# Performance work log

Hardware: AMD Instinct MI355X
Metric: run time of the kernel (lower is better)

## Reference

```python
import jax, jax.numpy as jnp
import numpy as np

N, E, G = 50000, 500000, 32
H, D = 4, 40  # heads, per-head dim; hidden = H*D = 160
HID, JK = H * D, 2 * H * D  # 160, 320


def setup_inputs() -> dict:
    key = jax.random.key(0)
    ks = jax.random.split(key, 32)
    s = 0.05
    inp = {
        'x': jax.random.normal(ks[0], (N, 5), jnp.float32),
        'edge_index': jax.random.randint(ks[1], (2, E), 0, N, jnp.int32).astype(jnp.int64),
        'edge_attr': jax.random.normal(ks[2], (E, 4), jnp.float32),
        'batch': jnp.sort(jax.random.randint(ks[3], (N,), 0, G, jnp.int32)).astype(jnp.int64),
        'W_in': jax.random.normal(ks[4], (5, HID), jnp.float32) * s,
        'b_in': jnp.zeros((HID,), jnp.float32),
        'Wq': jax.random.normal(ks[5], (2, HID, HID), jnp.float32) * s,
        'bq': jnp.zeros((2, HID), jnp.float32),
        'Wk': jax.random.normal(ks[6], (2, HID, HID), jnp.float32) * s,
        'bk': jnp.zeros((2, HID), jnp.float32),
        'Wv': jax.random.normal(ks[7], (2, HID, HID), jnp.float32) * s,
        'bv': jnp.zeros((2, HID), jnp.float32),
        'We': jax.random.normal(ks[8], (2, 4, HID), jnp.float32) * s,
        'be': jnp.zeros((2, HID), jnp.float32),
        'Wskip': jax.random.normal(ks[9], (2, HID, HID), jnp.float32) * s,
        'bskip': jnp.zeros((2, HID), jnp.float32),
        'Wbeta': jax.random.normal(ks[10], (2, 3 * HID, 1), jnp.float32) * s,
        'Wg1': jax.random.normal(ks[11], (JK, JK // 2), jnp.float32) * s,
        'bg1': jnp.zeros((JK // 2,), jnp.float32),
        'Wg2': jax.random.normal(ks[12], (JK // 2, 1), jnp.float32) * s,
        'bg2': jnp.zeros((1,), jnp.float32),
        'Wh1': jax.random.normal(ks[13], (JK, JK), jnp.float32) * s,
        'bh1': jnp.zeros((JK,), jnp.float32),
        'Wh2': jax.random.normal(ks[14], (JK, 6), jnp.float32) * s,
        'bh2': jnp.zeros((6,), jnp.float32),
    }
    return inp


def _transformer_conv(h, src, dst, edge_attr, Wq, bq, Wk, bk, Wv, bv, We, be, Wskip, bskip, Wbeta):
    n = h.shape[0]
    q = (h @ Wq + bq).reshape(n, H, D)
    k = (h @ Wk + bk).reshape(n, H, D)
    v = (h @ Wv + bv).reshape(n, H, D)
    e = (edge_attr @ We + be).reshape(-1, H, D)   # [E,H,D]
    k_e = k[src] + e                              # key with edge feature
    v_e = v[src] + e                              # value with edge feature
    alpha = jnp.einsum('ehd,ehd->eh', q[dst], k_e) / jnp.sqrt(jnp.float32(D))  # [E,H]
    # segment softmax over incoming edges of each destination node
    amax = jax.ops.segment_max(alpha, dst, num_segments=n)
    ex = jnp.exp(alpha - amax[dst])
    denom = jax.ops.segment_sum(ex, dst, num_segments=n)
    a = ex / denom[dst]                           # [E,H]
    out = jax.ops.segment_sum(v_e * a[..., None], dst, num_segments=n).reshape(n, H * D)
    # beta gate with skip connection
    r = h @ Wskip + bskip
    beta = jax.nn.sigmoid(jnp.concatenate([out, r, out - r], axis=-1) @ Wbeta)  # [n,1]
    return beta * r + (1.0 - beta) * out


def reference(x, edge_index, edge_attr, batch, W_in, b_in, Wq, bq, Wk, bk, Wv, bv,
              We, be, Wskip, bskip, Wbeta, Wg1, bg1, Wg2, bg2, Wh1, bh1, Wh2, bh2):
    src, dst = edge_index[0], edge_index[1]
    h = x @ W_in + b_in
    xs = []
    for l in range(2):
        h = _transformer_conv(h, src, dst, edge_attr, Wq[l], bq[l], Wk[l], bk[l],
                              Wv[l], bv[l], We[l], be[l], Wskip[l], bskip[l], Wbeta[l])
        xs.append(h)
    xc = jnp.concatenate(xs, axis=-1)             # JumpingKnowledge 'cat' -> [N,320]
    # AttentionalAggregation: gate MLP + segment softmax over graphs
    gate = jax.nn.relu(xc @ Wg1 + bg1) @ Wg2 + bg2  # [N,1]
    gmax = jax.ops.segment_max(gate, batch, num_segments=G)
    ge = jnp.exp(gate - gmax[batch])
    gden = jax.ops.segment_sum(ge, batch, num_segments=G)
    att = ge / gden[batch]
    pooled = jax.ops.segment_sum(att * xc, batch, num_segments=G)  # [G,320]
    out = jax.nn.relu(pooled @ Wh1 + bh1) @ Wh2 + bh2              # [G,6]
    return out.reshape(-1, 2, 3)
```

## Files before the change

kernel.cpp:

```cpp
#include <hip/hip_runtime.h>
#include <math.h>
#include <stddef.h>

#define NHEAD 4
#define DHEAD 40
#define HIDW 160
#define JKW 320
#define NGRAPH 32
#define BCAP 64

typedef __attribute__((ext_vector_type(8))) short short8;
typedef __attribute__((ext_vector_type(4))) float f32x4;
typedef __attribute__((ext_vector_type(2))) float f32x2;
typedef __fp16 h2 __attribute__((ext_vector_type(2)));
typedef int i32x4 __attribute__((ext_vector_type(4)));
typedef i32x4 i32x4_a4 __attribute__((aligned(4)));

__device__ inline unsigned short f2bf(float x){
  unsigned u = __float_as_uint(x);
  u += 0x7fff + ((u >> 16) & 1);
  return (unsigned short)(u >> 16);
}
__device__ inline float bf2f(unsigned short h){
  return __uint_as_float(((unsigned)h) << 16);
}
__device__ inline float fdot2(h2 a, h2 b, float c){
  return __builtin_amdgcn_fdot2(a, b, c, false);
}
__device__ inline h2 pk(float a, float b){
  return __builtin_amdgcn_cvt_pkrtz(a, b);
}
union HU { h2 h; int i; unsigned u; float f; };
__device__ inline h2 shfl_h2(h2 v, int xm){
  HU u; u.h = v; u.i = __shfl_xor(u.i, xm); return u.h;
}

#if __has_builtin(__builtin_amdgcn_cvt_pk_f16_fp8)
__device__ inline h2 cvt8(int s){ return __builtin_amdgcn_cvt_pk_f16_fp8((short)s); }
#else
__device__ inline h2 cvt8(int s){
  f32x2 t = __builtin_amdgcn_cvt_pk_f32_fp8(s, false);
  return pk(t.x, t.y);
}
#endif

__device__ inline int lbound(const int* __restrict__ b, int N, int g){
  int lo = 0, hi = N;
  while (lo < hi){ int mid = (lo + hi) >> 1; if (b[mid] < g) lo = mid + 1; else hi = mid; }
  return lo;
}

__global__ __launch_bounds__(256) void k_pre(const float* __restrict__ x, const float* __restrict__ W_in,
                                             const float* __restrict__ b_in, unsigned short* __restrict__ hb,
                                             const float* __restrict__ Wq, const float* __restrict__ Wk,
                                             const float* __restrict__ Wv, const float* __restrict__ Ws,
                                             const float* __restrict__ bq, const float* __restrict__ bk,
                                             const float* __restrict__ bv, const float* __restrict__ bs,
                                             const float* __restrict__ Wg1,
                                             unsigned short* __restrict__ Bth, float* __restrict__ bp,
                                             unsigned short* __restrict__ Btgh,
                                             int* __restrict__ cnt, float* __restrict__ gate,
                                             float* __restrict__ pooled, int N){
  int NL = (N*HIDW + 255)/256;
  int bid = blockIdx.x, tid = threadIdx.x;
  if (bid < NL){
    int idx = bid*256 + tid;
    if (idx >= N*HIDW) return;
    int n = idx / HIDW, j = idx % HIDW;
    const float* xr = x + n*5;
    float v = b_in[j];
    #pragma unroll
    for (int c = 0; c < 5; ++c) v += xr[c] * W_in[c*HIDW + j];
    hb[(size_t)n*JKW + j] = f2bf(v);
  } else if (bid < NL + 1005){
    int idx = (bid - NL)*256 + tid;
    if (idx < 204800){
      int l = idx / 102400, r = idx % 102400;
      int j = r / 160, i = r % 160;
      int sel = j / HIDW, jj = j % HIDW;
      const float* W = (sel==0) ? Wq : (sel==1) ? Wk : (sel==2) ? Wv : Ws;
      Bth[(size_t)l*102400 + (size_t)j*160 + i] = f2bf(W[(size_t)l*25600 + i*HIDW + jj]);
    } else if (idx < 256000){
      int r = idx - 204800;
      int j = r / 320, i = r % 320;
      Btgh[(size_t)j*320 + i] = f2bf(Wg1[(size_t)i*160 + j]);
    } else if (idx < 257280){
      int r = idx - 256000;
      int l = r / 640, j = r % 640;
      int sel = j / HIDW, jj = j % HIDW;
      const float* bb = (sel==0) ? bq : (sel==1) ? bk : (sel==2) ? bv : bs;
      bp[l*640 + j] = bb[l*160 + jj];
    }
  } else {
    int idx = (bid - NL - 1005)*256 + tid;
    if (idx < N){ cnt[idx] = 0; gate[idx] = 0.f; }
    if (idx < NGRAPH*JKW) pooled[idx] = 0.f;
  }
}

__global__ __launch_bounds__(256) void k_fill(const int* __restrict__ dst, const int* __restrict__ src,
                                              const float* __restrict__ edge_attr, int E,
                                              int* __restrict__ cnt, int* __restrict__ esrc,
                                              uint2* __restrict__ eattr){
  int e = blockIdx.x*256 + threadIdx.x;
  if (e < E){
    int d = dst[e];
    int p = atomicAdd(&cnt[d], 1);
    if (p < BCAP){
      int slot = d*BCAP + p;
      esrc[slot] = src[e];
      float4 ea = *(const float4*)(edge_attr + (size_t)e*4);
      HU a, b; a.h = pk(ea.x, ea.y); b.h = pk(ea.z, ea.w);
      eattr[slot] = make_uint2(a.u, b.u);
    }
  }
}

#define BSTR 40
#define BSTR1 164
template<int NSUB, int MODE>
__global__ __launch_bounds__(256) void k_mgemm(const unsigned short* __restrict__ A, int lda,
                                               const unsigned short* __restrict__ Bh,
                                               const float* __restrict__ bias,
                                               _Float16* __restrict__ qh,
                                               unsigned char* __restrict__ kv8,
                                               _Float16* __restrict__ rskip,
                                               const float* __restrict__ Wg2,
                                               float* __restrict__ gate,
                                               int M, int K){
  __shared__ short sBh[(MODE==1) ? (16*NSUB*BSTR1) : (2*16*NSUB*BSTR)];
  int tid = threadIdx.x;
  int wv = tid >> 6, lane = tid & 63;
  int quad = lane >> 4, l16 = lane & 15;

  int P = gridDim.x, MBy = gridDim.y;
  int bid = blockIdx.y * P + blockIdx.x;
  int fullRows = (MBy >> 3) << 3;
  int rowB, panel;
  if (bid < fullRows * P){
    int group = bid / (8*P), rem = bid % (8*P);
    rowB  = group*8 + (rem & 7);
    panel = rem >> 3;
  } else {
    int rem = bid - fullRows*P;
    int R = MBy - fullRows;
    panel = rem / R;
    rowB  = fullRows + rem % R;
  }
  int m0 = rowB*128 + wv*32;
  int col0 = panel * (16*NSUB);

  int ar0 = m0 + l16;      if (ar0 >= M) ar0 = M - 1;
  int ar1 = m0 + 16 + l16; if (ar1 >= M) ar1 = M - 1;
  const unsigned short* Ap0 = A + (size_t)ar0*lda + quad*8;
  const unsigned short* Ap1 = A + (size_t)ar1*lda + quad*8;

  f32x4 acc[2][NSUB];
  #pragma unroll
  for (int g = 0; g < 2; ++g)
    #pragma unroll
    for (int s = 0; s < NSUB; ++s) acc[g][s] = (f32x4){0.f,0.f,0.f,0.f};

  if constexpr (MODE == 1){
    for (int u = tid; u < 16*NSUB*20; u += 256){
      int col = u / 20, q = u % 20;
      *(short8*)(&sBh[col*BSTR1 + q*8]) =
        *(const short8*)(Bh + (size_t)(col0 + col)*K + q*8);
    }
    __syncthreads();
    #pragma unroll
    for (int kk = 0; kk < 5; ++kk){
      int k0 = kk << 5;
      short8 ah0 = *(const short8*)(Ap0 + k0);
      short8 ah1 = *(const short8*)(Ap1 + k0);
      #pragma unroll
      for (int s = 0; s < NSUB; ++s){
        short8 bh = *(const short8*)(&sBh[(s*16 + l16)*BSTR1 + k0 + quad*8]);
        acc[0][s] = __builtin_amdgcn_mfma_f32_16x16x32_bf16(ah0, bh, acc[0][s], 0, 0, 0);
        acc[1][s] = __builtin_amdgcn_mfma_f32_16x16x32_bf16(ah1, bh, acc[1][s], 0, 0, 0);
      }
    }
  } else {
    const int CH = K >> 5;
    for (int u = tid; u < 16*NSUB*4; u += 256){
      int col = u >> 2, q4 = u & 3;
      *(short8*)(&sBh[col*BSTR + q4*8]) =
        *(const short8*)(Bh + (size_t)(col0 + col)*K + q4*8);
    }
    __syncthreads();
    int buf = 0;
    for (int kk = 0; kk < CH; ++kk){
      int k0 = kk << 5;
      if (kk + 1 < CH){
        int kn = k0 + 32;
        for (int u = tid; u < 16*NSUB*4; u += 256){
          int col = u >> 2, q4 = u & 3;
          *(short8*)(&sBh[(buf^1)*16*NSUB*BSTR + col*BSTR + q4*8]) =
            *(const short8*)(Bh + (size_t)(col0 + col)*K + kn + q4*8);
        }
      }
      short8 ah0 = *(const short8*)(Ap0 + k0);
      short8 ah1 = *(const short8*)(Ap1 + k0);
      #pragma unroll
      for (int s = 0; s < NSUB; ++s){
        short8 bh = *(const short8*)(&sBh[buf*16*NSUB*BSTR + (s*16 + l16)*BSTR + quad*8]);
        acc[0][s] = __builtin_amdgcn_mfma_f32_16x16x32_bf16(ah0, bh, acc[0][s], 0, 0, 0);
        acc[1][s] = __builtin_amdgcn_mfma_f32_16x16x32_bf16(ah1, bh, acc[1][s], 0, 0, 0);
      }
      __syncthreads();
      buf ^= 1;
    }
  }

  const float qscale = 0.15811388300841898f;
  if (MODE == 1){
    #pragma unroll
    for (int g = 0; g < 2; ++g){
      #pragma unroll
      for (int s = 0; s < NSUB; ++s){
        int col = col0 + s*16 + l16;
        float bv = bias[col];
        int sel = col / 160, cc = col % 160;
        #pragma unroll
        for (int r = 0; r < 4; ++r){
          int row = m0 + g*16 + quad*4 + r;
          if (row >= M) continue;
          float v = acc[g][s][r] + bv;
          if (sel == 0)      qh[(size_t)row*160 + cc] = (_Float16)(v * qscale);
          else if (sel == 3) rskip[(size_t)row*160 + cc] = (_Float16)v;
          else {
            int slot = (cc/40)*4 + (cc%40)/10, j = cc%10;
            int e8 = __builtin_amdgcn_cvt_pk_fp8_f32(v, v, 0, false);
            kv8[(size_t)row*320 + slot*20 + (sel==2?10:0) + j] = (unsigned char)(e8 & 0xff);
          }
        }
      }
    }
  } else {
    float pg[2][4];
    #pragma unroll
    for (int g = 0; g < 2; ++g)
      #pragma unroll
      for (int r = 0; r < 4; ++r) pg[g][r] = 0.f;
    #pragma unroll
    for (int s = 0; s < NSUB; ++s){
      int col = col0 + s*16 + l16;
      float bv = bias[col], wg = Wg2[col];
      #pragma unroll
      for (int g = 0; g < 2; ++g)
        #pragma unroll
        for (int r = 0; r < 4; ++r)
          pg[g][r] += fmaxf(acc[g][s][r] + bv, 0.f) * wg;
    }
    #pragma unroll
    for (int g = 0; g < 2; ++g)
      #pragma unroll
      for (int r = 0; r < 4; ++r){
        float v = pg[g][r];
        v += __shfl_xor(v, 1); v += __shfl_xor(v, 2);
        v += __shfl_xor(v, 4); v += __shfl_xor(v, 8);
        int row = m0 + g*16 + quad*4 + r;
        if (l16 == 0 && row < M) atomicAdd(&gate[row], v);
      }
  }
}

__global__ __launch_bounds__(256) void k_qprep(const _Float16* __restrict__ qh,
                                               const float* __restrict__ We, const float* __restrict__ be,
                                               float* __restrict__ qwb, int N){
  int idx = blockIdx.x*256 + threadIdx.x;
  if (idx >= N*4) return;
  int n = idx >> 2, h = idx & 3;
  const _Float16* qp = qh + (size_t)n*160 + h*40;
  float w0=0.f,w1=0.f,w2=0.f,w3=0.f,b=0.f;
  #pragma unroll
  for (int d = 0; d < 40; ++d){
    float q = (float)qp[d];
    int c = h*40 + d;
    w0 += q*We[c];     w1 += q*We[160+c];
    w2 += q*We[320+c]; w3 += q*We[480+c];
    b  += q*be[c];
  }
  float* o = qwb + (size_t)idx*5;
  o[0]=w0; o[1]=w1; o[2]=w2; o[3]=w3; o[4]=b;
}

__global__ __launch_bounds__(256) void k_attn(const _Float16* __restrict__ qh,
                                              const unsigned char* __restrict__ kv8,
                                              const _Float16* __restrict__ rskip,
                                              const float* __restrict__ qwb,
                                              const uint2* __restrict__ eattr,
                                              const int* __restrict__ esrc,
                                              const int* __restrict__ cnt,
                                              const float* __restrict__ We, const float* __restrict__ be,
                                              const float* __restrict__ Wb,
                                              unsigned short* __restrict__ hb,
                                              int loff, int N){
  int n = blockIdx.x*4 + (threadIdx.x >> 6);
  if (n >= N) return;
  int lane = threadIdx.x & 63;
  int g4 = lane >> 4;
  int w  = lane & 15;
  int hh = w & 3, t = w >> 2;
  int cbase = DHEAD*hh + 10*t;
  int slot = hh*4 + t;

  h2 qh2[5];
  {
    const unsigned* qp = (const unsigned*)(qh + (size_t)n*160 + cbase);
    #pragma unroll
    for (int i = 0; i < 5; ++i){ HU u; u.u = qp[i]; qh2[i] = u.h; }
  }
  const float* qwp = qwb + ((size_t)n*4 + hh)*5;
  float qw0 = qwp[0], qw1 = qwp[1], qw2 = qwp[2], qw3 = qwp[3], qb = qwp[4];
  h2 qw01 = pk(qw0, qw1), qw23 = pk(qw2, qw3);

  float ssum = 0.f;
  h2 zh = pk(0.f, 0.f);
  h2 acch[5], sah[2];
  #pragma unroll
  for (int i = 0; i < 5; ++i) acch[i] = zh;
  sah[0] = zh; sah[1] = zh;

  int deg = cnt[n]; if (deg > BCAP) deg = BCAP;
  int st = n*BCAP, en = st + deg;
  int B = (deg + 3) >> 2;

  int snA=0, snB=0, snC=0; bool vA=false, vB=false, vC=false;
  h2 eaA0=zh, eaA1=zh, eaB0=zh, eaB1=zh, eaC0=zh, eaC1=zh;
  {
    int p0 = st + g4;       vA = (p0 < en);
    if (vA){ snA = esrc[p0]; uint2 e = eattr[p0]; HU a,b; a.u=e.x; b.u=e.y; eaA0=a.h; eaA1=b.h; }
    int p1 = st + 4 + g4;   vB = (p1 < en);
    if (vB){ snB = esrc[p1]; uint2 e = eattr[p1]; HU a,b; a.u=e.x; b.u=e.y; eaB0=a.h; eaB1=b.h; }
    int p2 = st + 8 + g4;   vC = (p2 < en);
    if (vC){ snC = esrc[p2]; uint2 e = eattr[p2]; HU a,b; a.u=e.x; b.u=e.y; eaC0=a.h; eaC1=b.h; }
  }
  i32x4 cA0 = {0,0,0,0}, cB0 = {0,0,0,0}; int cA4 = 0, cB4 = 0;
  if (vA){
    const unsigned char* kp = kv8 + (size_t)snA*320 + slot*20;
    cA0 = *(const i32x4_a4*)kp; cA4 = *(const int*)(kp+16);
  }
  if (vB){
    const unsigned char* kp = kv8 + (size_t)snB*320 + slot*20;
    cB0 = *(const i32x4_a4*)kp; cB4 = *(const int*)(kp+16);
  }

  for (int b = 0; b < B; ++b){
    int snD = 0; h2 eaD0 = zh, eaD1 = zh; bool vD;
    int p3 = st + (b+3)*4 + g4;
    vD = (p3 < en);
    if (vD){ snD = esrc[p3]; uint2 e = eattr[p3]; HU a,b2; a.u=e.x; b2.u=e.y; eaD0=a.h; eaD1=b2.h; }
    i32x4 cC0 = {0,0,0,0}; int cC4 = 0;
    if (vC){
      const unsigned char* kp = kv8 + (size_t)snC*320 + slot*20;
      cC0 = *(const i32x4_a4*)kp; cC4 = *(const int*)(kp+16);
    }
    float p = 0.f;
    if (vA){
      p = fdot2(qh2[0], cvt8(cA0.x), p);
      p = fdot2(qh2[1], cvt8(cA0.x >> 16), p);
      p = fdot2(qh2[2], cvt8(cA0.y), p);
      p = fdot2(qh2[3], cvt8(cA0.y >> 16), p);
      p = fdot2(qh2[4], cvt8(cA0.z), p);
    }
    p += __shfl_xor(p, 4);
    p += __shfl_xor(p, 8);
    p += qb;
    p = fdot2(eaA0, qw01, p);
    p = fdot2(eaA1, qw23, p);

    if (vA){
      float ex = __expf(p);
      ssum += ex;
      h2 eh = pk(ex, ex);
      acch[0] += cvt8(cA0.z >> 16)*eh;
      acch[1] += cvt8(cA0.w)*eh;
      acch[2] += cvt8(cA0.w >> 16)*eh;
      acch[3] += cvt8(cA4)*eh;
      acch[4] += cvt8(cA4 >> 16)*eh;
      sah[0] += eaA0*eh;
      sah[1] += eaA1*eh;
    }
    snA = snB; vA = vB; eaA0 = eaB0; eaA1 = eaB1; cA0 = cB0; cA4 = cB4;
    snB = snC; vB = vC; eaB0 = eaC0; eaB1 = eaC1; cB0 = cC0; cB4 = cC4;
    snC = snD; vC = vD; eaC0 = eaD0; eaC1 = eaD1;
  }

  #pragma unroll
  for (int xm = 16; xm < 64; xm <<= 1){
    ssum += __shfl_xor(ssum, xm);
    #pragma unroll
    for (int i = 0; i < 5; ++i) acch[i] += shfl_h2(acch[i], xm);
    sah[0] += shfl_h2(sah[0], xm);
    sah[1] += shfl_h2(sah[1], xm);
  }

  {
    float inv = (ssum > 0.f) ? 1.f/ssum : 0.f;
    float sw0 = (float)sah[0].x*inv, sw1 = (float)sah[0].y*inv;
    float sw2 = (float)sah[1].x*inv, sw3 = (float)sah[1].y*inv;
    float bterm = (ssum > 0.f) ? 1.f : 0.f;

    float a0 = (g4==0) ? (float)acch[0].x : (g4==1) ? (float)acch[0].y
             : (g4==2) ? (float)acch[1].x : (float)acch[1].y;
    float a1 = (g4==0) ? (float)acch[2].x : (g4==1) ? (float)acch[2].y
             : (g4==2) ? (float)acch[3].x : (float)acch[3].y;
    float a2 = (g4==0) ? (float)acch[4].x : (float)acch[4].y;

    const _Float16* rp = rskip + (size_t)n*160 + cbase;
    float ov[3], rrv[3];
    float part = 0.f;
    #pragma unroll
    for (int jj = 0; jj < 3; ++jj){
      int j = g4 + 4*jj;
      float aj = (jj==0) ? a0 : (jj==1) ? a1 : a2;
      ov[jj] = 0.f; rrv[jj] = 0.f;
      if (j < 10){
        int c = cbase + j;
        float o = aj*inv + sw0*We[c] + sw1*We[160+c] + sw2*We[320+c] + sw3*We[480+c] + bterm*be[c];
        float r = (float)rp[j];
        ov[jj] = o; rrv[jj] = r;
        part += o*Wb[c] + r*Wb[160+c] + (o-r)*Wb[320+c];
      }
    }
    #pragma unroll
    for (int xm = 1; xm < 64; xm <<= 1) part += __shfl_xor(part, xm);
    float beta = 1.f/(1.f + __expf(-part));
    unsigned short* hp = hb + (size_t)n*JKW + loff + cbase;
    #pragma unroll
    for (int jj = 0; jj < 3; ++jj){
      int j = g4 + 4*jj;
      if (j < 10) hp[j] = f2bf(beta*rrv[jj] + (1.f-beta)*ov[jj]);
    }
  }
}

__global__ __launch_bounds__(320) void k_pool(const unsigned short* __restrict__ hb, const float* __restrict__ gate,
                                              const int* __restrict__ batch, int N,
                                              float* __restrict__ pooled){
  __shared__ float sm[320];
  int g = blockIdx.x, part = blockIdx.y, j = threadIdx.x;
  int lo = lbound(batch, N, g), hi = lbound(batch, N, g+1);
  int len = hi - lo;
  if (len <= 0) return;
  float m = -INFINITY;
  for (int i = lo + j; i < hi; i += 320) m = fmaxf(m, gate[i]);
  sm[j] = m; __syncthreads();
  #pragma unroll
  for (int off = 256; off; off >>= 1){
    if (j < off && j + off < 320) sm[j] = fmaxf(sm[j], sm[j+off]);
    __syncthreads();
  }
  float gm = sm[0]; __syncthreads();
  float s = 0.f;
  for (int i = lo + j; i < hi; i += 320) s += __expf(gate[i] - gm);
  sm[j] = s; __syncthreads();
  #pragma unroll
  for (int off = 256; off; off >>= 1){
    if (j < off && j + off < 320) sm[j] += sm[j+off];
    __syncthreads();
  }
  float dg = sm[0];
  float invd = (dg > 0.f) ? 1.f/dg : 0.f;

  int chunk = (len + (int)gridDim.y - 1) / (int)gridDim.y;
  int a = lo + part*chunk;
  int bnd = a + chunk; if (bnd > hi) bnd = hi;
  if (a >= bnd) return;
  float acc = 0.f;
  for (int n = a; n < bnd; ++n){
    float at = __expf(gate[n] - gm);
    acc += at * bf2f(hb[(size_t)n*JKW + j]);
  }
  atomicAdd(&pooled[g*JKW + j], acc*invd);
}

__global__ __launch_bounds__(320) void k_head(const float* __restrict__ pooled, const float* __restrict__ Wh1,
                                              const float* __restrict__ bh1, const float* __restrict__ Wh2,
                                              const float* __restrict__ bh2, float* __restrict__ out){
  __shared__ float p[320];
  __shared__ float t[320];
  int g = blockIdx.x, tid = threadIdx.x;
  p[tid] = pooled[g*JKW + tid]; __syncthreads();
  float a = bh1[tid];
  for (int i = 0; i < 320; ++i) a += p[i]*Wh1[i*JKW + tid];
  t[tid] = fmaxf(a, 0.f); __syncthreads();
  if (tid < 6){
    float o = bh2[tid];
    for (int j = 0; j < 320; ++j) o += t[j]*Wh2[j*6 + tid];
    out[g*6 + tid] = o;
  }
}

extern "C" void kernel_launch(void* const* d_in, const int* in_sizes, int n_in,
                              void* d_out, int out_size, void* d_ws, size_t ws_size,
                              hipStream_t stream){
  (void)n_in; (void)out_size; (void)ws_size;
  const float* x        = (const float*)d_in[0];
  const int*   eidx     = (const int*)d_in[1];
  const float* edge_attr= (const float*)d_in[2];
  const int*   batch    = (const int*)d_in[3];
  const float* W_in     = (const float*)d_in[4];
  const float* b_in     = (const float*)d_in[5];
  const float* Wq       = (const float*)d_in[6];
  const float* bq       = (const float*)d_in[7];
  const float* Wk       = (const float*)d_in[8];
  const float* bk       = (const float*)d_in[9];
  const float* Wv       = (const float*)d_in[10];
  const float* bv       = (const float*)d_in[11];
  const float* We       = (const float*)d_in[12];
  const float* be       = (const float*)d_in[13];
  const float* Wsk      = (const float*)d_in[14];
  const float* bsk      = (const float*)d_in[15];
  const float* Wb       = (const float*)d_in[16];
  const float* Wg1      = (const float*)d_in[17];
  const float* bg1      = (const float*)d_in[18];
  const float* Wg2      = (const float*)d_in[19];
  const float* Wh1      = (const float*)d_in[21];
  const float* bh1      = (const float*)d_in[22];
  const float* Wh2      = (const float*)d_in[23];
  const float* bh2      = (const float*)d_in[24];

  const int N = in_sizes[0] / 5;
  const int E = in_sizes[1] / 2;
  float* out = (float*)d_out;

  char* w = (char*)d_ws;
  auto alloc = [&](size_t bytes)->char*{ char* p = w; w += (bytes + 255) & ~(size_t)255; return p; };
  unsigned short* hb = (unsigned short*)alloc((size_t)N*JKW*2);
  _Float16* qh  = (_Float16*)alloc((size_t)N*160*2);
  unsigned char* kv8 = (unsigned char*)alloc((size_t)N*320);
  _Float16* rskip = (_Float16*)alloc((size_t)N*160*2);
  float* qwb    = (float*)alloc((size_t)N*20*4);
  unsigned short* Bth  = (unsigned short*)alloc((size_t)2*640*160*2);
  unsigned short* Btgh = (unsigned short*)alloc((size_t)160*320*2);
  float* bpack  = (float*)alloc((size_t)2*640*4);
  int*   cnt    = (int*)alloc((size_t)N*4);
  int*   esrc   = (int*)alloc((size_t)N*BCAP*4);
  uint2* eattr  = (uint2*)alloc((size_t)N*BCAP*8);
  float* gate   = (float*)alloc((size_t)N*4);
  float* pooled = (float*)alloc(NGRAPH*JKW*4);

  const int* srcI = eidx;
  const int* dstI = eidx + E;

  const int NL = (N*HIDW + 255)/256;
  const int NZ = (N + 255)/256;
  k_pre<<<NL + 1005 + NZ, 256, 0, stream>>>(x, W_in, b_in, hb,
                                            Wq, Wk, Wv, Wsk, bq, bk, bv, bsk, Wg1,
                                            Bth, bpack, Btgh, cnt, gate, pooled, N);

  const int eb = (E + 255)/256;
  k_fill<<<eb, 256, 0, stream>>>(dstI, srcI, edge_attr, E, cnt, esrc, eattr);

  const int MB128 = (N + 127)/128;
  for (int l = 0; l < 2; ++l){
    dim3 g1(5, MB128);
    k_mgemm<8,1><<<g1, 256, 0, stream>>>(hb, JKW, Bth + (size_t)l*102400, bpack + l*640,
                                         qh, kv8, rskip, nullptr, nullptr, N, HIDW);
    k_qprep<<<(N*4 + 255)/256, 256, 0, stream>>>(qh, We + l*640, be + l*160, qwb, N);
    k_attn<<<(N + 3)/4, 256, 0, stream>>>(qh, kv8, rskip, qwb, eattr, esrc, cnt,
                                          We + l*640, be + l*160, Wb + l*480, hb, l*HIDW, N);
  }

  k_mgemm<10,2><<<dim3(1, MB128), 256, 0, stream>>>(hb, JKW, Btgh, bg1, nullptr, nullptr, nullptr,
                                                    Wg2, gate, N, JKW);

  dim3 g3(NGRAPH, 8);
  k_pool<<<g3, 320, 0, stream>>>(hb, gate, batch, N, pooled);
  k_head<<<NGRAPH, 320, 0, stream>>>(pooled, Wh1, bh1, Wh2, bh2, out);
}
```

Measured before the change: 492.1 us.

## Vectorize input projection stores, pair-load q in qprep, enlarge attention blocks

The input projection now has each thread compute 8 consecutive outputs, loading W_in with float4 and writing one 16-byte bf16 vector, which replaces scalar per-element stores. k_qprep reads q two halves at a time through 32-bit loads. k_attn moves from 4 to 8 nodes per 512-thread block, which cuts the block count but may change occupancy and scheduling.

```diff
diff --git a/kernel.cpp b/kernel.cpp
--- a/kernel.cpp
+++ b/kernel.cpp
@@ -61,17 +61,29 @@
                                              unsigned short* __restrict__ Btgh,
                                              int* __restrict__ cnt, float* __restrict__ gate,
                                              float* __restrict__ pooled, int N){
-  int NL = (N*HIDW + 255)/256;
+  int NL = (N*20 + 255)/256;
   int bid = blockIdx.x, tid = threadIdx.x;
   if (bid < NL){
     int idx = bid*256 + tid;
-    if (idx >= N*HIDW) return;
-    int n = idx / HIDW, j = idx % HIDW;
+    if (idx >= N*20) return;
+    int n = idx / 20, j8 = (idx % 20)*8;
     const float* xr = x + n*5;
-    float v = b_in[j];
-    #pragma unroll
-    for (int c = 0; c < 5; ++c) v += xr[c] * W_in[c*HIDW + j];
-    hb[(size_t)n*JKW + j] = f2bf(v);
+    float x0 = xr[0], x1 = xr[1], x2 = xr[2], x3 = xr[3], x4 = xr[4];
+    float v[8];
+    #pragma unroll
+    for (int u = 0; u < 8; ++u) v[u] = b_in[j8+u];
+    #pragma unroll
+    for (int c = 0; c < 5; ++c){
+      float xc = (c==0)?x0:(c==1)?x1:(c==2)?x2:(c==3)?x3:x4;
+      const float4 wa = *(const float4*)(W_in + c*HIDW + j8);
+      const float4 wb = *(const float4*)(W_in + c*HIDW + j8 + 4);
+      v[0] += xc*wa.x; v[1] += xc*wa.y; v[2] += xc*wa.z; v[3] += xc*wa.w;
+      v[4] += xc*wb.x; v[5] += xc*wb.y; v[6] += xc*wb.z; v[7] += xc*wb.w;
+    }
+    short8 o;
+    #pragma unroll
+    for (int u = 0; u < 8; ++u) o[u] = (short)f2bf(v[u]);
+    *(short8*)(hb + (size_t)n*JKW + j8) = o;
   } else if (bid < NL + 1005){
     int idx = (bid - NL)*256 + tid;
     if (idx < 204800){
@@ -271,21 +283,24 @@
   int idx = blockIdx.x*256 + threadIdx.x;
   if (idx >= N*4) return;
   int n = idx >> 2, h = idx & 3;
-  const _Float16* qp = qh + (size_t)n*160 + h*40;
+  const unsigned* qp = (const unsigned*)(qh + (size_t)n*160 + h*40);
   float w0=0.f,w1=0.f,w2=0.f,w3=0.f,b=0.f;
   #pragma unroll
-  for (int d = 0; d < 40; ++d){
-    float q = (float)qp[d];
-    int c = h*40 + d;
-    w0 += q*We[c];     w1 += q*We[160+c];
-    w2 += q*We[320+c]; w3 += q*We[480+c];
-    b  += q*be[c];
+  for (int i = 0; i < 20; ++i){
+    HU u; u.u = qp[i];
+    float qa = (float)u.h.x, qb = (float)u.h.y;
+    int c = h*40 + 2*i;
+    w0 += qa*We[c]       + qb*We[c+1];
+    w1 += qa*We[160+c]   + qb*We[161+c];
+    w2 += qa*We[320+c]   + qb*We[321+c];
+    w3 += qa*We[480+c]   + qb*We[481+c];
+    b  += qa*be[c]       + qb*be[c+1];
   }
   float* o = qwb + (size_t)idx*5;
   o[0]=w0; o[1]=w1; o[2]=w2; o[3]=w3; o[4]=b;
 }
 
-__global__ __launch_bounds__(256) void k_attn(const _Float16* __restrict__ qh,
+__global__ __launch_bounds__(512) void k_attn(const _Float16* __restrict__ qh,
                                               const unsigned char* __restrict__ kv8,
                                               const _Float16* __restrict__ rskip,
                                               const float* __restrict__ qwb,
@@ -296,7 +311,7 @@
                                               const float* __restrict__ Wb,
                                               unsigned short* __restrict__ hb,
                                               int loff, int N){
-  int n = blockIdx.x*4 + (threadIdx.x >> 6);
+  int n = blockIdx.x*8 + (threadIdx.x >> 6);
   if (n >= N) return;
   int lane = threadIdx.x & 63;
   int g4 = lane >> 4;
@@ -545,7 +560,7 @@
   const int* srcI = eidx;
   const int* dstI = eidx + E;
 
-  const int NL = (N*HIDW + 255)/256;
+  const int NL = (N*20 + 255)/256;
   const int NZ = (N + 255)/256;
   k_pre<<<NL + 1005 + NZ, 256, 0, stream>>>(x, W_in, b_in, hb,
                                             Wq, Wk, Wv, Wsk, bq, bk, bv, bsk, Wg1,
@@ -560,7 +575,7 @@
     k_mgemm<8,1><<<g1, 256, 0, stream>>>(hb, JKW, Bth + (size_t)l*102400, bpack + l*640,
                                          qh, kv8, rskip, nullptr, nullptr, N, HIDW);
     k_qprep<<<(N*4 + 255)/256, 256, 0, stream>>>(qh, We + l*640, be + l*160, qwb, N);
-    k_attn<<<(N + 3)/4, 256, 0, stream>>>(qh, kv8, rskip, qwb, eattr, esrc, cnt,
+    k_attn<<<(N + 7)/8, 512, 0, stream>>>(qh, kv8, rskip, qwb, eattr, esrc, cnt,
                                           We + l*640, be + l*160, Wb + l*480, hb, l*HIDW, N);
   }
 
```

Result: no change. 486.5 us (-1.1%).
